# Performance work log

Hardware: AMD Instinct MI355X
Metric: run time of the kernel (lower is better)

Reference implementation:

```python
import jax, jax.numpy as jnp
import numpy as np

V, D, H, L, S_MAX = 32000, 1024, 16, 4, 1024
HD = D // H          # head dim = 64
FF = 4 * D           # mlp hidden = 4096
B, S = 2, 1024


def _layernorm(x, w, b, eps=1e-5):
    mu = jnp.mean(x, axis=-1, keepdims=True)
    var = jnp.mean(jnp.square(x - mu), axis=-1, keepdims=True)
    return (x - mu) * jax.lax.rsqrt(var + eps) * w + b


def setup_inputs() -> dict:
    key = jax.random.key(0)
    ks = jax.random.split(key, 16)
    r = lambda k, shape: (jax.random.normal(k, shape, dtype=jnp.float32) * 0.02)
    return {
        "input_ids": jax.random.randint(ks[0], (B, S), 0, V),
        "tok_emb": r(ks[1], (V, D)),
        "pos_emb": r(ks[2], (S_MAX, D)),
        "ln1_w": jnp.ones((L, D)), "ln1_b": jnp.zeros((L, D)),
        "ln2_w": jnp.ones((L, D)), "ln2_b": jnp.zeros((L, D)),
        "q_w": r(ks[3], (L, D, D)), "q_b": jnp.zeros((L, D)),
        "k_w": r(ks[4], (L, D, D)), "k_b": jnp.zeros((L, D)),
        "v_w": r(ks[5], (L, D, D)), "v_b": jnp.zeros((L, D)),
        "o_w": r(ks[6], (L, D, D)), "o_b": jnp.zeros((L, D)),
        "fc1_w": r(ks[7], (L, FF, D)), "fc1_b": jnp.zeros((L, FF)),
        "fc2_w": r(ks[8], (L, D, FF)), "fc2_b": jnp.zeros((L, D)),
        "lnf_w": jnp.ones((D,)), "lnf_b": jnp.zeros((D,)),
        "head_w": r(ks[9], (V, D)),
    }


def reference(input_ids, tok_emb, pos_emb, ln1_w, ln1_b, ln2_w, ln2_b,
              q_w, q_b, k_w, k_b, v_w, v_b, o_w, o_b,
              fc1_w, fc1_b, fc2_w, fc2_b, lnf_w, lnf_b, head_w):
    b, s = input_ids.shape
    x = tok_emb[input_ids] + pos_emb[:s][None, :, :]          # [B,S,D]
    causal = jnp.tril(jnp.ones((s, s), dtype=bool))           # [S,S]
    scale = 1.0 / np.sqrt(HD)
    for i in range(L):
        # --- causal MHA block ---
        h = _layernorm(x, ln1_w[i], ln1_b[i])
        q = (h @ q_w[i].T + q_b[i]).reshape(b, s, H, HD)
        k = (h @ k_w[i].T + k_b[i]).reshape(b, s, H, HD)
        v = (h @ v_w[i].T + v_b[i]).reshape(b, s, H, HD)
        scores = jnp.einsum('bqhd,bkhd->bhqk', q, k) * scale  # [B,H,S,S]
        scores = jnp.where(causal[None, None], scores, -jnp.inf)
        attn = jax.nn.softmax(scores, axis=-1)
        y = jnp.einsum('bhqk,bkhd->bqhd', attn, v).reshape(b, s, D)
        x = x + (y @ o_w[i].T + o_b[i])
        # --- GELU MLP block (exact gelu, matching torch F.gelu default) ---
        h = _layernorm(x, ln2_w[i], ln2_b[i])
        h = jax.nn.gelu(h @ fc1_w[i].T + fc1_b[i], approximate=False)
        x = x + (h @ fc2_w[i].T + fc2_b[i])
    x = _layernorm(x, lnf_w, lnf_b)
    logits = x[:, -1, :] @ head_w.T                           # [B,V]
    return logits
```

## Files before the change

kernel.cpp:

```cpp
#include <hip/hip_runtime.h>

#define V_SIZE 32000
#define D_DIM  1024
#define H_HEADS 16
#define L_LAYERS 4
#define HD_DIM 64
#define FF_DIM 4096
#define B_BATCH 2
#define S_SEQ  1024
#define M_ROWS (B_BATCH*S_SEQ)
#define KSPL   2

typedef short  s16x8 __attribute__((ext_vector_type(8)));
typedef unsigned short u16x8 __attribute__((ext_vector_type(8)));
typedef float  f32x4 __attribute__((ext_vector_type(4)));
typedef unsigned short u16;
typedef unsigned int   u32;

__device__ inline u16 f2bf(float f){
    u32 u = __float_as_uint(f);
    return (u16)((u + 0x7FFFu + ((u >> 16) & 1u)) >> 16);
}
__device__ inline float b2f(u32 v){ return __uint_as_float(v << 16); }

__device__ inline float gelu_f(float v){
    float y = 0.7978845608f * (v + 0.044715f*v*v*v);
    y = fmaxf(-15.f, fminf(15.f, y));
    float u = __expf(-2.f*y);
    return v / (1.f + u);
}

__device__ inline char* lds_swz(void* base, int row, int byteoff){
    return (char*)base + row*128 + (byteoff ^ ((row & 7) << 4));
}

__device__ inline void gload16(const u16* g, u16* l){
    __builtin_amdgcn_global_load_lds(
        (const __attribute__((address_space(1))) void*)g,
        (__attribute__((address_space(3))) void*)l, 16, 0, 0);
}

__device__ inline int swz_src_col(int lin){
    int row = lin >> 3, s8 = lin & 7;
    return (s8*8) ^ ((row & 7) << 3);
}

__device__ inline s16x8 cvt8(float4 a, float4 b){
    s16x8 o;
    o[0]=(short)f2bf(a.x); o[1]=(short)f2bf(a.y);
    o[2]=(short)f2bf(a.z); o[3]=(short)f2bf(a.w);
    o[4]=(short)f2bf(b.x); o[5]=(short)f2bf(b.y);
    o[6]=(short)f2bf(b.z); o[7]=(short)f2bf(b.w);
    return o;
}

__global__ __launch_bounds__(256) void cvt_all_k(
    const float* __restrict__ qw, const float* __restrict__ kw,
    const float* __restrict__ vw, const float* __restrict__ ow,
    const float* __restrict__ f1w, const float* __restrict__ f2w,
    u16* __restrict__ w_qkv, u16* __restrict__ w_o,
    u16* __restrict__ w_f1, u16* __restrict__ w_f2)
{
    const long M1 = 1L << 20;
    const int bx = blockIdx.x;
    const float* s; u16* d; long base;
    if (bx < 3072){
        int which = bx >> 10;
        s = (which==0) ? qw : ((which==1) ? kw : vw);
        base = (long)(bx & 1023) * 4096;
        long layer = base >> 20, rem = base & (M1 - 1);
        d = w_qkv + layer*3*M1 + which*M1 + rem;
        s += base;
    } else if (bx < 4096){
        base = (long)(bx - 3072) * 4096; s = ow  + base; d = w_o  + base;
    } else if (bx < 8192){
        base = (long)(bx - 4096) * 4096; s = f1w + base; d = w_f1 + base;
    } else {
        base = (long)(bx - 8192) * 4096; s = f2w + base; d = w_f2 + base;
    }
    const int t8 = threadIdx.x * 8;
#pragma unroll
    for (int j = 0; j < 2; j++){
        const float* sp = s + j*2048 + t8;
        float4 v0 = *(const float4*)(sp);
        float4 v1 = *(const float4*)(sp + 4);
        *(s16x8*)(d + j*2048 + t8) = cvt8(v0, v1);
    }
}

__global__ __launch_bounds__(256) void embed_ln_k(
    const int* __restrict__ ids, const float* __restrict__ tok,
    const float* __restrict__ pos, const float* __restrict__ lw,
    const float* __restrict__ lb, float* __restrict__ x, u16* __restrict__ h)
{
    int row = blockIdx.x;
    int id  = ids[row];
    int s   = row & (S_SEQ - 1);
    int t   = threadIdx.x;
    float4 tv = *(const float4*)(tok + (size_t)id * D_DIM + t*4);
    float4 pv = *(const float4*)(pos + (size_t)s  * D_DIM + t*4);
    float4 vv;
    vv.x = tv.x + pv.x; vv.y = tv.y + pv.y; vv.z = tv.z + pv.z; vv.w = tv.w + pv.w;
    *(float4*)(x + (size_t)row * D_DIM + t*4) = vv;
    float sm  = vv.x + vv.y + vv.z + vv.w;
    float ss = vv.x*vv.x + vv.y*vv.y + vv.z*vv.z + vv.w*vv.w;
#pragma unroll
    for (int off = 1; off < 64; off <<= 1){
        sm += __shfl_xor(sm, off);
        ss += __shfl_xor(ss, off);
    }
    __shared__ float red[8];
    const int wid = t >> 6, lane = t & 63;
    if (lane == 0){ red[wid] = sm; red[4 + wid] = ss; }
    __syncthreads();
    sm = red[0] + red[1] + red[2] + red[3];
    ss = red[4] + red[5] + red[6] + red[7];
    float mu   = sm * (1.0f/1024.0f);
    float rstd = rsqrtf(ss * (1.0f/1024.0f) - mu*mu + 1e-5f);
    float4 wv = *(const float4*)(lw + t*4);
    float4 bv = *(const float4*)(lb + t*4);
    uint2 pk;
    pk.x = (u32)f2bf((vv.x-mu)*rstd*wv.x + bv.x) | ((u32)f2bf((vv.y-mu)*rstd*wv.y + bv.y) << 16);
    pk.y = (u32)f2bf((vv.z-mu)*rstd*wv.z + bv.z) | ((u32)f2bf((vv.w-mu)*rstd*wv.w + bv.w) << 16);
    *(uint2*)(h + (size_t)row * D_DIM + t*4) = pk;
}

__global__ __launch_bounds__(256) void ln_k(
    const float* __restrict__ x, const float* __restrict__ lw,
    const float* __restrict__ lb, u16* __restrict__ h)
{
    const int row = blockIdx.x, t = threadIdx.x;
    float4 a = *(const float4*)(x + (size_t)row * D_DIM + t*4);
    float sm = a.x + a.y + a.z + a.w;
    float ss = a.x*a.x + a.y*a.y + a.z*a.z + a.w*a.w;
#pragma unroll
    for (int o2 = 1; o2 < 64; o2 <<= 1){
        sm += __shfl_xor(sm, o2);
        ss += __shfl_xor(ss, o2);
    }
    __shared__ float red[8];
    const int wid = t >> 6, lane = t & 63;
    if (lane == 0){ red[wid] = sm; red[4 + wid] = ss; }
    __syncthreads();
    sm = red[0] + red[1] + red[2] + red[3];
    ss = red[4] + red[5] + red[6] + red[7];
    float mu   = sm * (1.0f/1024.0f);
    float rstd = rsqrtf(ss * (1.0f/1024.0f) - mu*mu + 1e-5f);
    float4 wv  = *(const float4*)(lw + t*4);
    float4 lbv = *(const float4*)(lb + t*4);
    uint2 pk;
    pk.x = (u32)f2bf((a.x-mu)*rstd*wv.x + lbv.x) | ((u32)f2bf((a.y-mu)*rstd*wv.y + lbv.y) << 16);
    pk.y = (u32)f2bf((a.z-mu)*rstd*wv.z + lbv.z) | ((u32)f2bf((a.w-mu)*rstd*wv.w + lbv.w) << 16);
    *(uint2*)(h + (size_t)row * D_DIM + t*4) = pk;
}

__global__ __launch_bounds__(256) void ln_pair_f_k(
    const float* __restrict__ x2, const float* __restrict__ w, const float* __restrict__ bb,
    float* __restrict__ outF)
{
    const int row = blockIdx.x, t = threadIdx.x;
    float4 vv = *(const float4*)(x2 + (size_t)row * D_DIM + t*4);
    float s  = vv.x + vv.y + vv.z + vv.w;
    float ss = vv.x*vv.x + vv.y*vv.y + vv.z*vv.z + vv.w*vv.w;
#pragma unroll
    for (int off = 1; off < 64; off <<= 1){
        s  += __shfl_xor(s,  off);
        ss += __shfl_xor(ss, off);
    }
    __shared__ float red[8];
    const int wid = t >> 6, lane = t & 63;
    if (lane == 0){ red[wid] = s; red[4 + wid] = ss; }
    __syncthreads();
    s  = red[0] + red[1] + red[2] + red[3];
    ss = red[4] + red[5] + red[6] + red[7];
    float mu   = s * (1.0f/1024.0f);
    float rstd = rsqrtf(ss * (1.0f/1024.0f) - mu*mu + 1e-5f);
    float4 wv = *(const float4*)(w  + t*4);
    float4 bv = *(const float4*)(bb + t*4);
    float4 o;
    o.x = (vv.x - mu)*rstd*wv.x + bv.x;
    o.y = (vv.y - mu)*rstd*wv.y + bv.y;
    o.z = (vv.z - mu)*rstd*wv.z + bv.z;
    o.w = (vv.w - mu)*rstd*wv.w + bv.w;
    *(float4*)(outF + (size_t)row * D_DIM + t*4) = o;
}

__global__ __launch_bounds__(256) void reduce_ln_k(
    const u16* __restrict__ part, const float* __restrict__ bias,
    float* __restrict__ x,
    const float* __restrict__ lw, const float* __restrict__ lb,
    u16* __restrict__ h)
{
    const int row = blockIdx.x, t = threadIdx.x;
    const size_t off = (size_t)row * D_DIM + t*4;
    float4 a = *(float4*)(x + off);
    float4 bv = *(const float4*)(bias + t*4);
    a.x += bv.x; a.y += bv.y; a.z += bv.z; a.w += bv.w;
#pragma unroll
    for (int si = 0; si < KSPL; si++){
        uint2 pv = *(const uint2*)(part + (size_t)si * M_ROWS * D_DIM + off);
        a.x += b2f(pv.x & 0xffffu); a.y += b2f(pv.x >> 16);
        a.z += b2f(pv.y & 0xffffu); a.w += b2f(pv.y >> 16);
    }
    *(float4*)(x + off) = a;
    float sm = a.x + a.y + a.z + a.w;
    float ss = a.x*a.x + a.y*a.y + a.z*a.z + a.w*a.w;
#pragma unroll
    for (int o2 = 1; o2 < 64; o2 <<= 1){
        sm += __shfl_xor(sm, o2);
        ss += __shfl_xor(ss, o2);
    }
    __shared__ float red[8];
    const int wid = t >> 6, lane = t & 63;
    if (lane == 0){ red[wid] = sm; red[4 + wid] = ss; }
    __syncthreads();
    sm = red[0] + red[1] + red[2] + red[3];
    ss = red[4] + red[5] + red[6] + red[7];
    float mu   = sm * (1.0f/1024.0f);
    float rstd = rsqrtf(ss * (1.0f/1024.0f) - mu*mu + 1e-5f);
    float4 wv = *(const float4*)(lw + t*4);
    float4 lbv = *(const float4*)(lb + t*4);
    uint2 pk;
    pk.x = (u32)f2bf((a.x-mu)*rstd*wv.x + lbv.x) | ((u32)f2bf((a.y-mu)*rstd*wv.y + lbv.y) << 16);
    pk.y = (u32)f2bf((a.z-mu)*rstd*wv.z + lbv.z) | ((u32)f2bf((a.w-mu)*rstd*wv.w + lbv.w) << 16);
    *(uint2*)(h + (size_t)row * D_DIM + t*4) = pk;
}

__global__ __launch_bounds__(256) void gemm_fc1_k(
    const u16* __restrict__ A, const u16* __restrict__ Bw,
    const float* __restrict__ b0, u16* __restrict__ outB, int Ndim, int Kdim)
{
    const int nx = gridDim.x, ny = gridDim.y;
    const int nwg = nx*ny;
    int orig = blockIdx.y*nx + blockIdx.x;
    int wg = (orig & 7)*(nwg >> 3) + (orig >> 3);
    const int bm = wg % nx;
    const int bn = wg / nx;

    const int nk = Kdim >> 6;

    __shared__ __align__(16) u16 As[2][128*64];
    __shared__ __align__(16) u16 Bs[2][128*64];

    const int t = threadIdx.x;
    const int wid = t >> 6, lane = t & 63, lr = lane & 15, lg = lane >> 4;
    const int wr = wid >> 1, wc = wid & 1;

    f32x4 acc[4][4];
#pragma unroll
    for (int m=0;m<4;m++)
#pragma unroll
        for (int n=0;n<4;n++) acc[m][n] = (f32x4){0.f,0.f,0.f,0.f};

    const u16* Abase = A  + (size_t)(bm*128)*Kdim;
    const u16* Bbase = Bw + (size_t)(bn*128)*Kdim;

    auto stage = [&](int koff, int buf){
#pragma unroll
        for (int i=0;i<4;i++){
            int lin = i*256 + t;
            int row = lin >> 3;
            int sc  = swz_src_col(lin);
            gload16(Abase + (size_t)row*Kdim + koff + sc, &As[buf][lin*8]);
        }
#pragma unroll
        for (int i=0;i<4;i++){
            int lin = i*256 + t;
            int row = lin >> 3;
            int sc  = swz_src_col(lin);
            gload16(Bbase + (size_t)row*Kdim + koff + sc, &Bs[buf][lin*8]);
        }
    };

    stage(0, 0);
    __syncthreads();
    int cb = 0;
    for (int ki = 0; ki < nk; ki++){
        if (ki+1 < nk) stage((ki+1)*64, cb^1);
#pragma unroll
        for (int kk=0;kk<2;kk++){
            s16x8 a[4], b[4];
#pragma unroll
            for (int m=0;m<4;m++)
                a[m] = *(s16x8*)lds_swz(As[cb], wr*64 + m*16 + lr, kk*64 + lg*16);
#pragma unroll
            for (int n=0;n<4;n++)
                b[n] = *(s16x8*)lds_swz(Bs[cb], wc*64 + n*16 + lr, kk*64 + lg*16);
#pragma unroll
            for (int m=0;m<4;m++)
#pragma unroll
                for (int n=0;n<4;n++)
                    acc[m][n] = __builtin_amdgcn_mfma_f32_16x16x32_bf16(a[m], b[n], acc[m][n], 0, 0, 0);
        }
        __syncthreads();
        cb ^= 1;
    }

#pragma unroll
    for (int n=0;n<4;n++){
        int col = bn*128 + wc*64 + n*16 + lr;
        float bvv = b0[col];
#pragma unroll
        for (int m=0;m<4;m++){
            int row0 = bm*128 + wr*64 + m*16 + lg*4;
#pragma unroll
            for (int j=0;j<4;j++){
                int row = row0 + j;
                float val = gelu_f(acc[m][n][j] + bvv);
                outB[(size_t)row * Ndim + col] = f2bf(val);
            }
        }
    }
}

__global__ __launch_bounds__(256) void gemm_qkv_k(
    const u16* __restrict__ A, const u16* __restrict__ Bw,
    const float* __restrict__ b0, const float* __restrict__ b1, const float* __restrict__ b2,
    u16* __restrict__ outB, int Ndim, int Kdim)
{
    const int nx = gridDim.x, ny = gridDim.y;
    const int nwg = nx*ny;
    int orig = blockIdx.y*nx + blockIdx.x;
    int wg = (orig & 7)*(nwg >> 3) + (orig >> 3);
    const int bm = wg % nx;
    const int bn = wg / nx;
    const int nk = Kdim >> 6;

    __shared__ __align__(16) u16 As[2][64*64];
    __shared__ __align__(16) u16 Bs[2][128*64];

    const int t = threadIdx.x;
    const int wid = t >> 6, lane = t & 63, lr = lane & 15, lg = lane >> 4;
    const int wr = wid >> 1, wc = wid & 1;

    f32x4 acc[2][4];
#pragma unroll
    for (int m=0;m<2;m++)
#pragma unroll
        for (int n=0;n<4;n++) acc[m][n] = (f32x4){0.f,0.f,0.f,0.f};

    const u16* Abase = A  + (size_t)(bm*64)*Kdim;
    const u16* Bbase = Bw + (size_t)(bn*128)*Kdim;

    auto stage = [&](int koff, int buf){
#pragma unroll
        for (int i=0;i<2;i++){
            int lin = i*256 + t;
            int row = lin >> 3;
            int sc  = swz_src_col(lin);
            gload16(Abase + (size_t)row*Kdim + koff + sc, &As[buf][lin*8]);
        }
#pragma unroll
        for (int i=0;i<4;i++){
            int lin = i*256 + t;
            int row = lin >> 3;
            int sc  = swz_src_col(lin);
            gload16(Bbase + (size_t)row*Kdim + koff + sc, &Bs[buf][lin*8]);
        }
    };

    stage(0, 0);
    __syncthreads();
    int cb = 0;
    for (int ki = 0; ki < nk; ki++){
        if (ki+1 < nk) stage((ki+1)*64, cb^1);
#pragma unroll
        for (int kk=0;kk<2;kk++){
            s16x8 a[2], b[4];
#pragma unroll
            for (int m=0;m<2;m++)
                a[m] = *(s16x8*)lds_swz(As[cb], wr*32 + m*16 + lr, kk*64 + lg*16);
#pragma unroll
            for (int n=0;n<4;n++)
                b[n] = *(s16x8*)lds_swz(Bs[cb], wc*64 + n*16 + lr, kk*64 + lg*16);
#pragma unroll
            for (int m=0;m<2;m++)
#pragma unroll
                for (int n=0;n<4;n++)
                    acc[m][n] = __builtin_amdgcn_mfma_f32_16x16x32_bf16(a[m], b[n], acc[m][n], 0, 0, 0);
        }
        __syncthreads();
        cb ^= 1;
    }

#pragma unroll
    for (int n=0;n<4;n++){
        int col = bn*128 + wc*64 + n*16 + lr;
        int which = col >> 10;
        const float* bp = (which==0) ? b0 : ((which==1) ? b1 : b2);
        float bvv = bp[col & 1023];
        float scl = (which == 0) ? 0.125f : 1.0f;
#pragma unroll
        for (int m=0;m<2;m++){
            int row0 = bm*64 + wr*32 + m*16 + lg*4;
#pragma unroll
            for (int j=0;j<4;j++){
                int row = row0 + j;
                float val = (acc[m][n][j] + bvv) * scl;
                outB[(size_t)row * Ndim + col] = f2bf(val);
            }
        }
    }
}

__global__ __launch_bounds__(256) void gemm64_k(
    const u16* __restrict__ A, const u16* __restrict__ Bw,
    u16* __restrict__ outP, int Ndim, int Kdim, int kper)
{
    const int nx = gridDim.x, ny = gridDim.y;
    const int nwg = nx*ny*gridDim.z;
    int orig = (blockIdx.z*ny + blockIdx.y)*nx + blockIdx.x;
    int wg = (orig & 7)*(nwg >> 3) + (orig >> 3);
    const int bm = wg % nx; wg /= nx;
    const int bn = wg % ny;
    const int z  = wg / ny;
    const int kbeg = z * kper;
    const int nk = kper >> 6;

    __shared__ __align__(16) u16 As[2][64*64];
    __shared__ __align__(16) u16 Bs[2][128*64];

    const int t = threadIdx.x;
    const int wid = t >> 6, lane = t & 63, lr = lane & 15, lg = lane >> 4;
    const int wr = wid >> 1, wc = wid & 1;

    f32x4 acc[2][4];
#pragma unroll
    for (int m=0;m<2;m++)
#pragma unroll
        for (int n=0;n<4;n++) acc[m][n] = (f32x4){0.f,0.f,0.f,0.f};

    const u16* Abase = A  + (size_t)(bm*64)*Kdim + kbeg;
    const u16* Bbase = Bw + (size_t)(bn*128)*Kdim + kbeg;

    auto stage = [&](int koff, int buf){
#pragma unroll
        for (int i=0;i<2;i++){
            int lin = i*256 + t;
            int row = lin >> 3;
            int sc  = swz_src_col(lin);
            gload16(Abase + (size_t)row*Kdim + koff + sc, &As[buf][lin*8]);
        }
#pragma unroll
        for (int i=0;i<4;i++){
            int lin = i*256 + t;
            int row = lin >> 3;
            int sc  = swz_src_col(lin);
            gload16(Bbase + (size_t)row*Kdim + koff + sc, &Bs[buf][lin*8]);
        }
    };

    stage(0, 0);
    __syncthreads();
    int cb = 0;
    for (int ki = 0; ki < nk; ki++){
        if (ki+1 < nk) stage((ki+1)*64, cb^1);
#pragma unroll
        for (int kk=0;kk<2;kk++){
            s16x8 a[2], b[4];
#pragma unroll
            for (int m=0;m<2;m++)
                a[m] = *(s16x8*)lds_swz(As[cb], wr*32 + m*16 + lr, kk*64 + lg*16);
#pragma unroll
            for (int n=0;n<4;n++)
                b[n] = *(s16x8*)lds_swz(Bs[cb], wc*64 + n*16 + lr, kk*64 + lg*16);
#pragma unroll
            for (int m=0;m<2;m++)
#pragma unroll
                for (int n=0;n<4;n++)
                    acc[m][n] = __builtin_amdgcn_mfma_f32_16x16x32_bf16(a[m], b[n], acc[m][n], 0, 0, 0);
        }
        __syncthreads();
        cb ^= 1;
    }

#pragma unroll
    for (int n=0;n<4;n++){
        int col = bn*128 + wc*64 + n*16 + lr;
#pragma unroll
        for (int m=0;m<2;m++){
            int row0 = bm*64 + wr*32 + m*16 + lg*4;
#pragma unroll
            for (int j=0;j<4;j++){
                int row = row0 + j;
                outP[(size_t)z * M_ROWS * Ndim + (size_t)row * Ndim + col] = f2bf(acc[m][n][j]);
            }
        }
    }
}

__global__ __launch_bounds__(256) void attn_k(
    const u16* __restrict__ qkv, u16* __restrict__ y)
{
    const int gx = gridDim.x;
    const int nwg = gx * gridDim.y;
    int orig = blockIdx.y*gx + blockIdx.x;
    int wg = (orig & 7)*(nwg >> 3) + (orig >> 3);
    const int p  = wg % gx;
    const int bh = wg / gx;
    const int b  = bh >> 4, h = bh & 15;

    const int s_lo = p, s_hi = 15 - p;
    const int ntiles = s_hi + 1;

    __shared__ __align__(16) u16 Ks[2][64*64];
    __shared__ __align__(16) u16 VTs[2][64*64];
    __shared__ __align__(16) u16 Ps[4][16*64];

    const int t = threadIdx.x, wid = t >> 6, lane = t & 63, lr = lane & 15, lg = lane >> 4;
    const size_t rowb = (size_t)b * S_SEQ;
    const u16* qp = qkv + h*HD_DIM;
    const u16* kp = qkv + 1024 + h*HD_DIM;
    const u16* vp = qkv + 2048 + h*HD_DIM;

    const int qw_lo = s_lo*64 + wid*16;
    const int qw_hi = s_hi*64 + wid*16;

    s16x8 aq_lo[2], aq_hi[2];
#pragma unroll
    for (int kc=0;kc<2;kc++){
        aq_lo[kc] = *(const s16x8*)(qp + (rowb + qw_lo + lr) * 3072 + kc*32 + lg*8);
        aq_hi[kc] = *(const s16x8*)(qp + (rowb + qw_hi + lr) * 3072 + kc*32 + lg*8);
    }

    f32x4 o_lo[4], o_hi[4];
#pragma unroll
    for (int n=0;n<4;n++){ o_lo[n] = (f32x4){0.f,0.f,0.f,0.f}; o_hi[n] = (f32x4){0.f,0.f,0.f,0.f}; }
    float l_lo[4] = {0.f,0.f,0.f,0.f}, l_hi[4] = {0.f,0.f,0.f,0.f};

    const int kpr = t >> 3, dsl = t & 7;
    u16x8 vr0, vr1;

    auto issueK = [&](int kt, int buf){
#pragma unroll
        for (int i=0;i<2;i++){
            int lin = i*256 + t;
            int row = lin >> 3;
            int sc  = swz_src_col(lin);
            gload16(kp + (rowb + kt*64 + row)*3072 + sc, &Ks[buf][lin*8]);
        }
    };
    auto loadV = [&](int kt){
        vr0 = *(const u16x8*)(vp + (rowb + kt*64 + 2*kpr    )*3072 + dsl*8);
        vr1 = *(const u16x8*)(vp + (rowb + kt*64 + 2*kpr + 1)*3072 + dsl*8);
    };
    auto writeVT = [&](int buf){
#pragma unroll
        for (int j=0;j<8;j++){
            u32 pk = (u32)vr0[j] | ((u32)vr1[j] << 16);
            *(u32*)lds_swz(VTs[buf], dsl*8 + j, kpr*4) = pk;
        }
    };

    auto doStrip = [&](const s16x8* aq, f32x4* o, float* lsum, int qwS, int kt, bool diag, int cb){
        f32x4 sf[4];
#pragma unroll
        for (int n=0;n<4;n++) sf[n] = (f32x4){0.f,0.f,0.f,0.f};
        __builtin_amdgcn_s_setprio(1);
#pragma unroll
        for (int kc=0;kc<2;kc++){
#pragma unroll
            for (int n=0;n<4;n++){
                s16x8 bk = *(s16x8*)lds_swz(Ks[cb], n*16 + lr, kc*64 + lg*16);
                sf[n] = __builtin_amdgcn_mfma_f32_16x16x32_bf16(aq[kc], bk, sf[n], 0, 0, 0);
            }
        }
        __builtin_amdgcn_s_setprio(0);
        float rs[4] = {0.f,0.f,0.f,0.f};
#pragma unroll
        for (int n=0;n<4;n++){
            int key = kt*64 + n*16 + lr;
#pragma unroll
            for (int j=0;j<4;j++){
                float pe = __expf(sf[n][j]);
                if (diag && key > qwS + lg*4 + j) pe = 0.f;
                sf[n][j] = pe; rs[j] += pe;
            }
        }
#pragma unroll
        for (int off=1; off<16; off<<=1){
#pragma unroll
            for (int j=0;j<4;j++) rs[j] += __shfl_xor(rs[j], off);
        }
#pragma unroll
        for (int j=0;j<4;j++) lsum[j] += rs[j];
        u16* Pw = Ps[wid];
#pragma unroll
        for (int n=0;n<4;n++)
#pragma unroll
            for (int j=0;j<4;j++)
                *(u16*)lds_swz(Pw, lg*4 + j, (n*16 + lr)*2) = f2bf(sf[n][j]);
        __builtin_amdgcn_s_setprio(1);
#pragma unroll
        for (int kc=0;kc<2;kc++){
            s16x8 pa = *(s16x8*)lds_swz(Pw, lr, kc*64 + lg*16);
#pragma unroll
            for (int n=0;n<4;n++){
                s16x8 bv = *(s16x8*)lds_swz(VTs[cb], n*16 + lr, kc*64 + lg*16);
                o[n] = __builtin_amdgcn_mfma_f32_16x16x32_bf16(pa, bv, o[n], 0, 0, 0);
            }
        }
        __builtin_amdgcn_s_setprio(0);
    };

    issueK(0, 0); loadV(0); writeVT(0);
    __syncthreads();
    int cb = 0;
    for (int kt = 0; kt < ntiles; kt++){
        const bool more = (kt+1 < ntiles);
        if (more){ issueK(kt+1, cb^1); loadV(kt+1); }

        doStrip(aq_hi, o_hi, l_hi, qw_hi, kt, kt == s_hi, cb);
        if (kt <= s_lo)
            doStrip(aq_lo, o_lo, l_lo, qw_lo, kt, kt == s_lo, cb);

        if (more) writeVT(cb^1);
        __syncthreads();
        cb ^= 1;
    }

    float inv_lo[4], inv_hi[4];
#pragma unroll
    for (int j=0;j<4;j++){ inv_lo[j] = 1.0f / l_lo[j]; inv_hi[j] = 1.0f / l_hi[j]; }
#pragma unroll
    for (int n=0;n<4;n++)
#pragma unroll
        for (int j=0;j<4;j++){
            y[(rowb + qw_hi + lg*4 + j) * D_DIM + h*HD_DIM + n*16 + lr] = f2bf(o_hi[n][j] * inv_hi[j]);
            y[(rowb + qw_lo + lg*4 + j) * D_DIM + h*HD_DIM + n*16 + lr] = f2bf(o_lo[n][j] * inv_lo[j]);
        }
}

__global__ __launch_bounds__(256) void attn_last_k(
    const u16* __restrict__ qkv, float* __restrict__ Yp, float* __restrict__ psp)
{
    const int chunk = blockIdx.x;
    const int bh = blockIdx.y;
    const int b = bh >> 4, h = bh & 15;
    const int t = threadIdx.x;
    const size_t rowb = (size_t)b * S_SEQ;
    const size_t qrow = rowb + S_SEQ - 1;
    __shared__ float qs[64];
    __shared__ float ps[256];
    __shared__ float red[4];
    __shared__ float yred[4][64];
    if (t < 64) qs[t] = b2f(qkv[qrow*3072 + h*HD_DIM + t]);
    __syncthreads();
    int k = chunk*256 + t;
    const u16* krow = qkv + (rowb + k)*3072 + 1024 + h*HD_DIM;
    float s = 0.f;
#pragma unroll
    for (int j=0;j<8;j++){
        u16x8 kv = *(const u16x8*)(krow + j*8);
#pragma unroll
        for (int e=0;e<8;e++) s += qs[j*8+e] * b2f((u32)(unsigned short)kv[e]);
    }
    float p = __expf(s);
    ps[t] = p;
    float sp_ = p;
#pragma unroll
    for (int off=1; off<64; off<<=1) sp_ += __shfl_xor(sp_, off);
    if ((t & 63) == 0) red[t>>6] = sp_;
    __syncthreads();
    if (t == 0) psp[chunk*32 + bh] = red[0]+red[1]+red[2]+red[3];
    int d = t & 63, c = t >> 6;
    float acc = 0.f;
    const u16* vbase = qkv + (rowb + chunk*256 + c*64)*3072 + 2048 + h*HD_DIM + d;
    for (int kk=0; kk<64; kk++)
        acc += ps[c*64 + kk] * b2f((u32)vbase[(size_t)kk*3072]);
    yred[c][d] = acc;
    __syncthreads();
    if (t < 64)
        Yp[(chunk*32 + bh)*64 + t] = yred[0][t]+yred[1][t]+yred[2][t]+yred[3][t];
}

__global__ __launch_bounds__(64) void attn_comb_k(
    const float* __restrict__ Yp, const float* __restrict__ psp, u16* __restrict__ y2)
{
    int bh = blockIdx.x, t = threadIdx.x;
    float psum = psp[bh] + psp[32+bh] + psp[64+bh] + psp[96+bh];
    float y = Yp[bh*64+t] + Yp[(32+bh)*64+t] + Yp[(64+bh)*64+t] + Yp[(96+bh)*64+t];
    int b = bh >> 4, h = bh & 15;
    y2[b*1024 + h*64 + t] = f2bf(y / psum);
}

template<int MODE>
__global__ __launch_bounds__(256) void rowpair_k(
    const u16* __restrict__ A2, const u16* __restrict__ W,
    const float* __restrict__ bias, const float* __restrict__ xin,
    float* __restrict__ outF, u16* __restrict__ outB,
    int Ndim, int Kdim)
{
    const int t = threadIdx.x, wid = t >> 6, lane = t & 63;
    const int colsPerBlock = Ndim >> 8;
    const int colsPerWave  = colsPerBlock >> 2;
    const int nj = Kdim >> 9;
    for (int cc = 0; cc < colsPerWave; cc++){
        int col = blockIdx.x * colsPerBlock + wid * colsPerWave + cc;
        const u16* wrow = W + (size_t)col * Kdim;
        float s0 = 0.f, s1 = 0.f;
        for (int j = 0; j < nj; j++){
            int k = j*512 + lane*8;
            u16x8 wv = *(const u16x8*)(wrow + k);
            u16x8 a0 = *(const u16x8*)(A2 + k);
            u16x8 a1 = *(const u16x8*)(A2 + Kdim + k);
#pragma unroll
            for (int e=0;e<8;e++){
                float wf = b2f((u32)wv[e]);
                s0 += b2f((u32)a0[e]) * wf;
                s1 += b2f((u32)a1[e]) * wf;
            }
        }
#pragma unroll
        for (int off=1; off<64; off<<=1){
            s0 += __shfl_xor(s0, off);
            s1 += __shfl_xor(s1, off);
        }
        if (lane == 0){
            float bv = bias[col];
            if (MODE == 0){
                outF[col]         = xin[(size_t)(S_SEQ-1)*D_DIM + col]   + bv + s0;
                outF[D_DIM + col] = xin[(size_t)(2*S_SEQ-1)*D_DIM + col] + bv + s1;
            } else if (MODE == 1){
                outB[col]         = f2bf(gelu_f(s0 + bv));
                outB[Ndim + col]  = f2bf(gelu_f(s1 + bv));
            } else {
                outF[col]         = xin[col]         + bv + s0;
                outF[D_DIM + col] = xin[D_DIM + col] + bv + s1;
            }
        }
    }
}

__global__ __launch_bounds__(256) void head_k(
    const float* __restrict__ xf, const float* __restrict__ hw, float* __restrict__ out)
{
    __shared__ float xs[2*D_DIM];
    int t = threadIdx.x;
#pragma unroll
    for (int i=0;i<2;i++){
        int j = t + i*256;
        *(float4*)&xs[j*4] = *(const float4*)(xf + j*4);
    }
    __syncthreads();
    int wid = t >> 6, lane = t & 63;
    int vrow = blockIdx.x * 4 + wid;
    float s0 = 0.f, s1 = 0.f;
#pragma unroll
    for (int it=0; it<4; it++){
        int j = it*64 + lane;
        float4 w4 = *(const float4*)(hw + (size_t)vrow * D_DIM + j*4);
        float4 x0 = *(const float4*)&xs[j*4];
        float4 x1 = *(const float4*)&xs[D_DIM + j*4];
        s0 += w4.x*x0.x + w4.y*x0.y + w4.z*x0.z + w4.w*x0.w;
        s1 += w4.x*x1.x + w4.y*x1.y + w4.z*x1.z + w4.w*x1.w;
    }
#pragma unroll
    for (int off=1; off<64; off<<=1){
        s0 += __shfl_xor(s0, off);
        s1 += __shfl_xor(s1, off);
    }
    if (lane == 0){
        out[vrow]          = s0;
        out[V_SIZE + vrow] = s1;
    }
}

extern "C" void kernel_launch(void* const* d_in, const int* in_sizes, int n_in,
                              void* d_out, int out_size, void* d_ws, size_t ws_size,
                              hipStream_t stream)
{
    (void)in_sizes; (void)n_in; (void)out_size; (void)ws_size;
    const int*   ids  = (const int*)  d_in[0];
    const float* tok  = (const float*)d_in[1];
    const float* pos  = (const float*)d_in[2];
    const float* ln1w = (const float*)d_in[3];
    const float* ln1b = (const float*)d_in[4];
    const float* ln2w = (const float*)d_in[5];
    const float* ln2b = (const float*)d_in[6];
    const float* qw   = (const float*)d_in[7];
    const float* qbi  = (const float*)d_in[8];
    const float* kw   = (const float*)d_in[9];
    const float* kbi  = (const float*)d_in[10];
    const float* vw   = (const float*)d_in[11];
    const float* vbi  = (const float*)d_in[12];
    const float* ow   = (const float*)d_in[13];
    const float* obi  = (const float*)d_in[14];
    const float* f1w  = (const float*)d_in[15];
    const float* f1b  = (const float*)d_in[16];
    const float* f2w  = (const float*)d_in[17];
    const float* f2b  = (const float*)d_in[18];
    const float* lnfw = (const float*)d_in[19];
    const float* lnfb = (const float*)d_in[20];
    const float* hw   = (const float*)d_in[21];

    const long MD = (long)1024*1024;
    char* p = (char*)d_ws;
    float* x    = (float*)p; p += (size_t)M_ROWS * D_DIM * 4;
    u16* h      = (u16*)p;   p += (size_t)M_ROWS * D_DIM * 2;
    u16* qkvbuf = (u16*)p;   p += (size_t)M_ROWS * 3072 * 2;
    u16* ybuf   = (u16*)p;   p += (size_t)M_ROWS * D_DIM * 2;
    u16* h1     = (u16*)p;   p += (size_t)M_ROWS * FF_DIM * 2;
    u16* part   = (u16*)p;   p += (size_t)KSPL * M_ROWS * D_DIM * 2;
    u16* wbuf   = (u16*)p;   p += (size_t)48 * MD * 2;
    float* xf   = (float*)p; p += 2 * D_DIM * 4;
    u16*   y2   = (u16*)p;   p += 2 * D_DIM * 2;
    float* x2   = (float*)p; p += 2 * D_DIM * 4;
    float* x3   = (float*)p; p += 2 * D_DIM * 4;
    u16*   h2   = (u16*)p;   p += 2 * D_DIM * 2;
    u16*   g2   = (u16*)p;   p += 2 * FF_DIM * 2;
    float* Yp   = (float*)p; p += 4 * 32 * 64 * 4;
    float* psp  = (float*)p; p += 4 * 32 * 4;
    float* logits = (float*)d_out;

    u16* w_qkv = wbuf;
    u16* w_o   = wbuf + 12*MD;
    u16* w_f1  = wbuf + 16*MD;
    u16* w_f2  = wbuf + 32*MD;

    cvt_all_k<<<dim3(12288), 256, 0, stream>>>(
        qw, kw, vw, ow, f1w, f2w, w_qkv, w_o, w_f1, w_f2);

    embed_ln_k<<<dim3(M_ROWS), 256, 0, stream>>>(ids, tok, pos, ln1w, ln1b, x, h);

    for (int i = 0; i < L_LAYERS - 1; i++){
        gemm_qkv_k<<<dim3(32, 24), 256, 0, stream>>>(
            h, w_qkv + (size_t)i*3*MD,
            qbi + i*D_DIM, kbi + i*D_DIM, vbi + i*D_DIM,
            qkvbuf, 3072, D_DIM);
        attn_k<<<dim3(8, 32), 256, 0, stream>>>(qkvbuf, ybuf);
        gemm64_k<<<dim3(32, 8, KSPL), 256, 0, stream>>>(
            ybuf, w_o + (size_t)i*MD, part, D_DIM, D_DIM, D_DIM/KSPL);
        reduce_ln_k<<<dim3(M_ROWS), 256, 0, stream>>>(
            part, obi + i*D_DIM, x, ln2w + i*D_DIM, ln2b + i*D_DIM, h);
        gemm_fc1_k<<<dim3(16, 32), 256, 0, stream>>>(
            h, w_f1 + (size_t)i*4*MD, f1b + i*FF_DIM, h1, FF_DIM, D_DIM);
        gemm64_k<<<dim3(32, 8, KSPL), 256, 0, stream>>>(
            h1, w_f2 + (size_t)i*4*MD, part, D_DIM, FF_DIM, FF_DIM/KSPL);
        reduce_ln_k<<<dim3(M_ROWS), 256, 0, stream>>>(
            part, f2b + i*D_DIM, x, ln1w + (i+1)*D_DIM, ln1b + (i+1)*D_DIM, h);
    }

    const int L3 = L_LAYERS - 1;
    gemm_qkv_k<<<dim3(32, 24), 256, 0, stream>>>(
        h, w_qkv + (size_t)L3*3*MD,
        qbi + L3*D_DIM, kbi + L3*D_DIM, vbi + L3*D_DIM,
        qkvbuf, 3072, D_DIM);
    attn_last_k<<<dim3(4, 32), 256, 0, stream>>>(qkvbuf, Yp, psp);
    attn_comb_k<<<dim3(32), 64, 0, stream>>>(Yp, psp, y2);
    rowpair_k<0><<<dim3(256), 256, 0, stream>>>(
        y2, w_o + (size_t)L3*MD, obi + L3*D_DIM, x, x2, nullptr, D_DIM, D_DIM);
    ln_k<<<dim3(2), 256, 0, stream>>>(x2, ln2w + L3*D_DIM, ln2b + L3*D_DIM, h2);
    rowpair_k<1><<<dim3(256), 256, 0, stream>>>(
        h2, w_f1 + (size_t)L3*4*MD, f1b + L3*FF_DIM, nullptr, nullptr, g2, FF_DIM, D_DIM);
    rowpair_k<2><<<dim3(256), 256, 0, stream>>>(
        g2, w_f2 + (size_t)L3*4*MD, f2b + L3*D_DIM, x2, x3, nullptr, D_DIM, FF_DIM);
    ln_pair_f_k<<<dim3(2), 256, 0, stream>>>(x3, lnfw, lnfb, xf);

    head_k<<<dim3(V_SIZE/4), 256, 0, stream>>>(xf, hw, logits);
}
```

Baseline: 533.6 us.

## Fuse last-layer small kernels and compute only K/V for final layer

Removes the separate ln_k, attn_comb_k and ln_pair_f_k kernels by folding their work into the rowpair and head kernels. The head kernel now recomputes the final layernorm for both rows in every block. The final layer's QKV GEMM now computes only K and V, and Q for the two last rows comes from a rowpair GEMV. FC1 now uses the templated 64-row-tile GEMM instead of the 128x128 kernel. This cuts launches and skips most of the final-layer Q projection, at the cost of redundant per-block layernorm work in the head kernel.

```diff
diff --git a/kernel.cpp b/kernel.cpp
--- a/kernel.cpp
+++ b/kernel.cpp
@@ -125,66 +125,6 @@
     *(uint2*)(h + (size_t)row * D_DIM + t*4) = pk;
 }
 
-__global__ __launch_bounds__(256) void ln_k(
-    const float* __restrict__ x, const float* __restrict__ lw,
-    const float* __restrict__ lb, u16* __restrict__ h)
-{
-    const int row = blockIdx.x, t = threadIdx.x;
-    float4 a = *(const float4*)(x + (size_t)row * D_DIM + t*4);
-    float sm = a.x + a.y + a.z + a.w;
-    float ss = a.x*a.x + a.y*a.y + a.z*a.z + a.w*a.w;
-#pragma unroll
-    for (int o2 = 1; o2 < 64; o2 <<= 1){
-        sm += __shfl_xor(sm, o2);
-        ss += __shfl_xor(ss, o2);
-    }
-    __shared__ float red[8];
-    const int wid = t >> 6, lane = t & 63;
-    if (lane == 0){ red[wid] = sm; red[4 + wid] = ss; }
-    __syncthreads();
-    sm = red[0] + red[1] + red[2] + red[3];
-    ss = red[4] + red[5] + red[6] + red[7];
-    float mu   = sm * (1.0f/1024.0f);
-    float rstd = rsqrtf(ss * (1.0f/1024.0f) - mu*mu + 1e-5f);
-    float4 wv  = *(const float4*)(lw + t*4);
-    float4 lbv = *(const float4*)(lb + t*4);
-    uint2 pk;
-    pk.x = (u32)f2bf((a.x-mu)*rstd*wv.x + lbv.x) | ((u32)f2bf((a.y-mu)*rstd*wv.y + lbv.y) << 16);
-    pk.y = (u32)f2bf((a.z-mu)*rstd*wv.z + lbv.z) | ((u32)f2bf((a.w-mu)*rstd*wv.w + lbv.w) << 16);
-    *(uint2*)(h + (size_t)row * D_DIM + t*4) = pk;
-}
-
-__global__ __launch_bounds__(256) void ln_pair_f_k(
-    const float* __restrict__ x2, const float* __restrict__ w, const float* __restrict__ bb,
-    float* __restrict__ outF)
-{
-    const int row = blockIdx.x, t = threadIdx.x;
-    float4 vv = *(const float4*)(x2 + (size_t)row * D_DIM + t*4);
-    float s  = vv.x + vv.y + vv.z + vv.w;
-    float ss = vv.x*vv.x + vv.y*vv.y + vv.z*vv.z + vv.w*vv.w;
-#pragma unroll
-    for (int off = 1; off < 64; off <<= 1){
-        s  += __shfl_xor(s,  off);
-        ss += __shfl_xor(ss, off);
-    }
-    __shared__ float red[8];
-    const int wid = t >> 6, lane = t & 63;
-    if (lane == 0){ red[wid] = s; red[4 + wid] = ss; }
-    __syncthreads();
-    s  = red[0] + red[1] + red[2] + red[3];
-    ss = red[4] + red[5] + red[6] + red[7];
-    float mu   = s * (1.0f/1024.0f);
-    float rstd = rsqrtf(ss * (1.0f/1024.0f) - mu*mu + 1e-5f);
-    float4 wv = *(const float4*)(w  + t*4);
-    float4 bv = *(const float4*)(bb + t*4);
-    float4 o;
-    o.x = (vv.x - mu)*rstd*wv.x + bv.x;
-    o.y = (vv.y - mu)*rstd*wv.y + bv.y;
-    o.z = (vv.z - mu)*rstd*wv.z + bv.z;
-    o.w = (vv.w - mu)*rstd*wv.w + bv.w;
-    *(float4*)(outF + (size_t)row * D_DIM + t*4) = o;
-}
-
 __global__ __launch_bounds__(256) void reduce_ln_k(
     const u16* __restrict__ part, const float* __restrict__ bias,
     float* __restrict__ x,
@@ -226,94 +166,8 @@
     *(uint2*)(h + (size_t)row * D_DIM + t*4) = pk;
 }
 
-__global__ __launch_bounds__(256) void gemm_fc1_k(
-    const u16* __restrict__ A, const u16* __restrict__ Bw,
-    const float* __restrict__ b0, u16* __restrict__ outB, int Ndim, int Kdim)
-{
-    const int nx = gridDim.x, ny = gridDim.y;
-    const int nwg = nx*ny;
-    int orig = blockIdx.y*nx + blockIdx.x;
-    int wg = (orig & 7)*(nwg >> 3) + (orig >> 3);
-    const int bm = wg % nx;
-    const int bn = wg / nx;
-
-    const int nk = Kdim >> 6;
-
-    __shared__ __align__(16) u16 As[2][128*64];
-    __shared__ __align__(16) u16 Bs[2][128*64];
-
-    const int t = threadIdx.x;
-    const int wid = t >> 6, lane = t & 63, lr = lane & 15, lg = lane >> 4;
-    const int wr = wid >> 1, wc = wid & 1;
-
-    f32x4 acc[4][4];
-#pragma unroll
-    for (int m=0;m<4;m++)
-#pragma unroll
-        for (int n=0;n<4;n++) acc[m][n] = (f32x4){0.f,0.f,0.f,0.f};
-
-    const u16* Abase = A  + (size_t)(bm*128)*Kdim;
-    const u16* Bbase = Bw + (size_t)(bn*128)*Kdim;
-
-    auto stage = [&](int koff, int buf){
-#pragma unroll
-        for (int i=0;i<4;i++){
-            int lin = i*256 + t;
-            int row = lin >> 3;
-            int sc  = swz_src_col(lin);
-            gload16(Abase + (size_t)row*Kdim + koff + sc, &As[buf][lin*8]);
-        }
-#pragma unroll
-        for (int i=0;i<4;i++){
-            int lin = i*256 + t;
-            int row = lin >> 3;
-            int sc  = swz_src_col(lin);
-            gload16(Bbase + (size_t)row*Kdim + koff + sc, &Bs[buf][lin*8]);
-        }
-    };
-
-    stage(0, 0);
-    __syncthreads();
-    int cb = 0;
-    for (int ki = 0; ki < nk; ki++){
-        if (ki+1 < nk) stage((ki+1)*64, cb^1);
-#pragma unroll
-        for (int kk=0;kk<2;kk++){
-            s16x8 a[4], b[4];
-#pragma unroll
-            for (int m=0;m<4;m++)
-                a[m] = *(s16x8*)lds_swz(As[cb], wr*64 + m*16 + lr, kk*64 + lg*16);
-#pragma unroll
-            for (int n=0;n<4;n++)
-                b[n] = *(s16x8*)lds_swz(Bs[cb], wc*64 + n*16 + lr, kk*64 + lg*16);
-#pragma unroll
-            for (int m=0;m<4;m++)
-#pragma unroll
-                for (int n=0;n<4;n++)
-                    acc[m][n] = __builtin_amdgcn_mfma_f32_16x16x32_bf16(a[m], b[n], acc[m][n], 0, 0, 0);
-        }
-        __syncthreads();
-        cb ^= 1;
-    }
-
-#pragma unroll
-    for (int n=0;n<4;n++){
-        int col = bn*128 + wc*64 + n*16 + lr;
-        float bvv = b0[col];
-#pragma unroll
-        for (int m=0;m<4;m++){
-            int row0 = bm*128 + wr*64 + m*16 + lg*4;
-#pragma unroll
-            for (int j=0;j<4;j++){
-                int row = row0 + j;
-                float val = gelu_f(acc[m][n][j] + bvv);
-                outB[(size_t)row * Ndim + col] = f2bf(val);
-            }
-        }
-    }
-}
-
-__global__ __launch_bounds__(256) void gemm_qkv_k(
+template<int EPI, int QSEG>
+__global__ __launch_bounds__(256) void gemm64o_k(
     const u16* __restrict__ A, const u16* __restrict__ Bw,
     const float* __restrict__ b0, const float* __restrict__ b1, const float* __restrict__ b2,
     u16* __restrict__ outB, int Ndim, int Kdim)
@@ -386,17 +240,24 @@
 #pragma unroll
     for (int n=0;n<4;n++){
         int col = bn*128 + wc*64 + n*16 + lr;
-        int which = col >> 10;
-        const float* bp = (which==0) ? b0 : ((which==1) ? b1 : b2);
-        float bvv = bp[col & 1023];
-        float scl = (which == 0) ? 0.125f : 1.0f;
+        float bvv, scl = 1.0f;
+        if (EPI == 1){
+            bvv = b0[col];
+        } else {
+            int which = col >> 10;
+            const float* bp = (which==0) ? b0 : ((which==1) ? b1 : b2);
+            bvv = bp[col & 1023];
+            if (which == QSEG) scl = 0.125f;
+        }
 #pragma unroll
         for (int m=0;m<2;m++){
             int row0 = bm*64 + wr*32 + m*16 + lg*4;
 #pragma unroll
             for (int j=0;j<4;j++){
                 int row = row0 + j;
-                float val = (acc[m][n][j] + bvv) * scl;
+                float val = acc[m][n][j] + bvv;
+                if (EPI == 1) val = gelu_f(val);
+                else          val *= scl;
                 outB[(size_t)row * Ndim + col] = f2bf(val);
             }
         }
@@ -632,28 +493,28 @@
 }
 
 __global__ __launch_bounds__(256) void attn_last_k(
-    const u16* __restrict__ qkv, float* __restrict__ Yp, float* __restrict__ psp)
+    const u16* __restrict__ q2, const u16* __restrict__ kv,
+    float* __restrict__ Yp, float* __restrict__ psp)
 {
     const int chunk = blockIdx.x;
     const int bh = blockIdx.y;
     const int b = bh >> 4, h = bh & 15;
     const int t = threadIdx.x;
     const size_t rowb = (size_t)b * S_SEQ;
-    const size_t qrow = rowb + S_SEQ - 1;
     __shared__ float qs[64];
     __shared__ float ps[256];
     __shared__ float red[4];
     __shared__ float yred[4][64];
-    if (t < 64) qs[t] = b2f(qkv[qrow*3072 + h*HD_DIM + t]);
+    if (t < 64) qs[t] = b2f(q2[b*1024 + h*HD_DIM + t]);
     __syncthreads();
     int k = chunk*256 + t;
-    const u16* krow = qkv + (rowb + k)*3072 + 1024 + h*HD_DIM;
+    const u16* krow = kv + (rowb + k)*2048 + h*HD_DIM;
     float s = 0.f;
 #pragma unroll
     for (int j=0;j<8;j++){
-        u16x8 kv = *(const u16x8*)(krow + j*8);
-#pragma unroll
-        for (int e=0;e<8;e++) s += qs[j*8+e] * b2f((u32)(unsigned short)kv[e]);
+        u16x8 kv8 = *(const u16x8*)(krow + j*8);
+#pragma unroll
+        for (int e=0;e<8;e++) s += qs[j*8+e] * b2f((u32)(unsigned short)kv8[e]);
     }
     float p = __expf(s);
     ps[t] = p;
@@ -665,33 +526,70 @@
     if (t == 0) psp[chunk*32 + bh] = red[0]+red[1]+red[2]+red[3];
     int d = t & 63, c = t >> 6;
     float acc = 0.f;
-    const u16* vbase = qkv + (rowb + chunk*256 + c*64)*3072 + 2048 + h*HD_DIM + d;
+    const u16* vbase = kv + (rowb + chunk*256 + c*64)*2048 + 1024 + h*HD_DIM + d;
     for (int kk=0; kk<64; kk++)
-        acc += ps[c*64 + kk] * b2f((u32)vbase[(size_t)kk*3072]);
+        acc += ps[c*64 + kk] * b2f((u32)vbase[(size_t)kk*2048]);
     yred[c][d] = acc;
     __syncthreads();
     if (t < 64)
         Yp[(chunk*32 + bh)*64 + t] = yred[0][t]+yred[1][t]+yred[2][t]+yred[3][t];
 }
 
-__global__ __launch_bounds__(64) void attn_comb_k(
-    const float* __restrict__ Yp, const float* __restrict__ psp, u16* __restrict__ y2)
-{
-    int bh = blockIdx.x, t = threadIdx.x;
-    float psum = psp[bh] + psp[32+bh] + psp[64+bh] + psp[96+bh];
-    float y = Yp[bh*64+t] + Yp[(32+bh)*64+t] + Yp[(64+bh)*64+t] + Yp[(96+bh)*64+t];
-    int b = bh >> 4, h = bh & 15;
-    y2[b*1024 + h*64 + t] = f2bf(y / psum);
-}
-
 template<int MODE>
 __global__ __launch_bounds__(256) void rowpair_k(
-    const u16* __restrict__ A2, const u16* __restrict__ W,
-    const float* __restrict__ bias, const float* __restrict__ xin,
+    const u16* __restrict__ A0, const u16* __restrict__ A1,
+    const float* __restrict__ Yp, const float* __restrict__ psp,
+    const float* __restrict__ x2in,
+    const float* __restrict__ lw, const float* __restrict__ lb,
+    const u16* __restrict__ W, const float* __restrict__ bias,
+    const float* __restrict__ xresid,
     float* __restrict__ outF, u16* __restrict__ outB,
     int Ndim, int Kdim)
 {
+    __shared__ u16 As16[2][1024];
+    __shared__ float red[8];
     const int t = threadIdx.x, wid = t >> 6, lane = t & 63;
+
+    if (MODE == 0){
+        for (int idx = t; idx < 2048; idx += 256){
+            int r = idx >> 10, d10 = idx & 1023;
+            int bh = r*16 + (d10 >> 6), d = d10 & 63;
+            float psum = psp[bh] + psp[32+bh] + psp[64+bh] + psp[96+bh];
+            float yv = Yp[bh*64+d] + Yp[(32+bh)*64+d] + Yp[(64+bh)*64+d] + Yp[(96+bh)*64+d];
+            As16[r][d10] = f2bf(yv / psum);
+        }
+        __syncthreads();
+    }
+    if (MODE == 1){
+#pragma unroll
+        for (int r = 0; r < 2; r++){
+            float4 vv = *(const float4*)(x2in + r*1024 + t*4);
+            float sm = vv.x + vv.y + vv.z + vv.w;
+            float ss = vv.x*vv.x + vv.y*vv.y + vv.z*vv.z + vv.w*vv.w;
+#pragma unroll
+            for (int o2 = 1; o2 < 64; o2 <<= 1){
+                sm += __shfl_xor(sm, o2);
+                ss += __shfl_xor(ss, o2);
+            }
+            if (lane == 0){ red[wid] = sm; red[4+wid] = ss; }
+            __syncthreads();
+            sm = red[0]+red[1]+red[2]+red[3];
+            ss = red[4]+red[5]+red[6]+red[7];
+            float mu = sm * (1.0f/1024.0f);
+            float rstd = rsqrtf(ss * (1.0f/1024.0f) - mu*mu + 1e-5f);
+            float4 wv  = *(const float4*)(lw + t*4);
+            float4 lbv = *(const float4*)(lb + t*4);
+            As16[r][t*4+0] = f2bf((vv.x-mu)*rstd*wv.x + lbv.x);
+            As16[r][t*4+1] = f2bf((vv.y-mu)*rstd*wv.y + lbv.y);
+            As16[r][t*4+2] = f2bf((vv.z-mu)*rstd*wv.z + lbv.z);
+            As16[r][t*4+3] = f2bf((vv.w-mu)*rstd*wv.w + lbv.w);
+            __syncthreads();
+        }
+    }
+
+    const u16* pa0 = (MODE==0 || MODE==1) ? (const u16*)As16[0] : A0;
+    const u16* pa1 = (MODE==0 || MODE==1) ? (const u16*)As16[1] : A1;
+
     const int colsPerBlock = Ndim >> 8;
     const int colsPerWave  = colsPerBlock >> 2;
     const int nj = Kdim >> 9;
@@ -702,8 +600,8 @@
         for (int j = 0; j < nj; j++){
             int k = j*512 + lane*8;
             u16x8 wv = *(const u16x8*)(wrow + k);
-            u16x8 a0 = *(const u16x8*)(A2 + k);
-            u16x8 a1 = *(const u16x8*)(A2 + Kdim + k);
+            u16x8 a0 = *(const u16x8*)(pa0 + k);
+            u16x8 a1 = *(const u16x8*)(pa1 + k);
 #pragma unroll
             for (int e=0;e<8;e++){
                 float wf = b2f((u32)wv[e]);
@@ -719,31 +617,53 @@
         if (lane == 0){
             float bv = bias[col];
             if (MODE == 0){
-                outF[col]         = xin[(size_t)(S_SEQ-1)*D_DIM + col]   + bv + s0;
-                outF[D_DIM + col] = xin[(size_t)(2*S_SEQ-1)*D_DIM + col] + bv + s1;
+                outF[col]         = xresid[(size_t)(S_SEQ-1)*D_DIM + col]   + bv + s0;
+                outF[D_DIM + col] = xresid[(size_t)(2*S_SEQ-1)*D_DIM + col] + bv + s1;
             } else if (MODE == 1){
                 outB[col]         = f2bf(gelu_f(s0 + bv));
                 outB[Ndim + col]  = f2bf(gelu_f(s1 + bv));
+            } else if (MODE == 2){
+                outF[col]         = x2in[col]         + bv + s0;
+                outF[D_DIM + col] = x2in[D_DIM + col] + bv + s1;
             } else {
-                outF[col]         = xin[col]         + bv + s0;
-                outF[D_DIM + col] = xin[D_DIM + col] + bv + s1;
+                outB[col]         = f2bf((s0 + bv) * 0.125f);
+                outB[Ndim + col]  = f2bf((s1 + bv) * 0.125f);
             }
         }
     }
 }
 
-__global__ __launch_bounds__(256) void head_k(
-    const float* __restrict__ xf, const float* __restrict__ hw, float* __restrict__ out)
+__global__ __launch_bounds__(256) void head_ln_k(
+    const float* __restrict__ x3, const float* __restrict__ w, const float* __restrict__ bb,
+    const float* __restrict__ hw, float* __restrict__ out)
 {
     __shared__ float xs[2*D_DIM];
-    int t = threadIdx.x;
-#pragma unroll
-    for (int i=0;i<2;i++){
-        int j = t + i*256;
-        *(float4*)&xs[j*4] = *(const float4*)(xf + j*4);
-    }
-    __syncthreads();
-    int wid = t >> 6, lane = t & 63;
+    __shared__ float red[8];
+    int t = threadIdx.x, wid = t >> 6, lane = t & 63;
+#pragma unroll
+    for (int r = 0; r < 2; r++){
+        float4 vv = *(const float4*)(x3 + r*D_DIM + t*4);
+        float s  = vv.x + vv.y + vv.z + vv.w;
+        float ss = vv.x*vv.x + vv.y*vv.y + vv.z*vv.z + vv.w*vv.w;
+#pragma unroll
+        for (int off = 1; off < 64; off <<= 1){
+            s  += __shfl_xor(s,  off);
+            ss += __shfl_xor(ss, off);
+        }
+        if (lane == 0){ red[wid] = s; red[4+wid] = ss; }
+        __syncthreads();
+        s  = red[0]+red[1]+red[2]+red[3];
+        ss = red[4]+red[5]+red[6]+red[7];
+        float mu   = s * (1.0f/1024.0f);
+        float rstd = rsqrtf(ss * (1.0f/1024.0f) - mu*mu + 1e-5f);
+        float4 wv = *(const float4*)(w  + t*4);
+        float4 bv = *(const float4*)(bb + t*4);
+        xs[r*D_DIM + t*4+0] = (vv.x-mu)*rstd*wv.x + bv.x;
+        xs[r*D_DIM + t*4+1] = (vv.y-mu)*rstd*wv.y + bv.y;
+        xs[r*D_DIM + t*4+2] = (vv.z-mu)*rstd*wv.z + bv.z;
+        xs[r*D_DIM + t*4+3] = (vv.w-mu)*rstd*wv.w + bv.w;
+        __syncthreads();
+    }
     int vrow = blockIdx.x * 4 + wid;
     float s0 = 0.f, s1 = 0.f;
 #pragma unroll
@@ -803,11 +723,9 @@
     u16* h1     = (u16*)p;   p += (size_t)M_ROWS * FF_DIM * 2;
     u16* part   = (u16*)p;   p += (size_t)KSPL * M_ROWS * D_DIM * 2;
     u16* wbuf   = (u16*)p;   p += (size_t)48 * MD * 2;
-    float* xf   = (float*)p; p += 2 * D_DIM * 4;
-    u16*   y2   = (u16*)p;   p += 2 * D_DIM * 2;
+    u16*   q2   = (u16*)p;   p += 2 * D_DIM * 2;
     float* x2   = (float*)p; p += 2 * D_DIM * 4;
     float* x3   = (float*)p; p += 2 * D_DIM * 4;
-    u16*   h2   = (u16*)p;   p += 2 * D_DIM * 2;
     u16*   g2   = (u16*)p;   p += 2 * FF_DIM * 2;
     float* Yp   = (float*)p; p += 4 * 32 * 64 * 4;
     float* psp  = (float*)p; p += 4 * 32 * 4;
@@ -824,7 +742,7 @@
     embed_ln_k<<<dim3(M_ROWS), 256, 0, stream>>>(ids, tok, pos, ln1w, ln1b, x, h);
 
     for (int i = 0; i < L_LAYERS - 1; i++){
-        gemm_qkv_k<<<dim3(32, 24), 256, 0, stream>>>(
+        gemm64o_k<0,0><<<dim3(32, 24), 256, 0, stream>>>(
             h, w_qkv + (size_t)i*3*MD,
             qbi + i*D_DIM, kbi + i*D_DIM, vbi + i*D_DIM,
             qkvbuf, 3072, D_DIM);
@@ -833,8 +751,10 @@
             ybuf, w_o + (size_t)i*MD, part, D_DIM, D_DIM, D_DIM/KSPL);
         reduce_ln_k<<<dim3(M_ROWS), 256, 0, stream>>>(
             part, obi + i*D_DIM, x, ln2w + i*D_DIM, ln2b + i*D_DIM, h);
-        gemm_fc1_k<<<dim3(16, 32), 256, 0, stream>>>(
-            h, w_f1 + (size_t)i*4*MD, f1b + i*FF_DIM, h1, FF_DIM, D_DIM);
+        gemm64o_k<1,-1><<<dim3(32, 32), 256, 0, stream>>>(
+            h, w_f1 + (size_t)i*4*MD,
+            f1b + i*FF_DIM, nullptr, nullptr,
+            h1, FF_DIM, D_DIM);
         gemm64_k<<<dim3(32, 8, KSPL), 256, 0, stream>>>(
             h1, w_f2 + (size_t)i*4*MD, part, D_DIM, FF_DIM, FF_DIM/KSPL);
         reduce_ln_k<<<dim3(M_ROWS), 256, 0, stream>>>(
@@ -842,20 +762,28 @@
     }
 
     const int L3 = L_LAYERS - 1;
-    gemm_qkv_k<<<dim3(32, 24), 256, 0, stream>>>(
-        h, w_qkv + (size_t)L3*3*MD,
-        qbi + L3*D_DIM, kbi + L3*D_DIM, vbi + L3*D_DIM,
-        qkvbuf, 3072, D_DIM);
-    attn_last_k<<<dim3(4, 32), 256, 0, stream>>>(qkvbuf, Yp, psp);
-    attn_comb_k<<<dim3(32), 64, 0, stream>>>(Yp, psp, y2);
+    gemm64o_k<0,-1><<<dim3(32, 16), 256, 0, stream>>>(
+        h, w_qkv + (size_t)L3*3*MD + MD,
+        kbi + L3*D_DIM, vbi + L3*D_DIM, vbi + L3*D_DIM,
+        qkvbuf, 2048, D_DIM);
+    rowpair_k<3><<<dim3(256), 256, 0, stream>>>(
+        h + (size_t)(S_SEQ-1)*D_DIM, h + (size_t)(2*S_SEQ-1)*D_DIM,
+        nullptr, nullptr, nullptr, nullptr, nullptr,
+        w_qkv + (size_t)L3*3*MD, qbi + L3*D_DIM, nullptr,
+        nullptr, q2, D_DIM, D_DIM);
+    attn_last_k<<<dim3(4, 32), 256, 0, stream>>>(q2, qkvbuf, Yp, psp);
     rowpair_k<0><<<dim3(256), 256, 0, stream>>>(
-        y2, w_o + (size_t)L3*MD, obi + L3*D_DIM, x, x2, nullptr, D_DIM, D_DIM);
-    ln_k<<<dim3(2), 256, 0, stream>>>(x2, ln2w + L3*D_DIM, ln2b + L3*D_DIM, h2);
+        nullptr, nullptr, Yp, psp, nullptr, nullptr, nullptr,
+        w_o + (size_t)L3*MD, obi + L3*D_DIM, x,
+        x2, nullptr, D_DIM, D_DIM);
     rowpair_k<1><<<dim3(256), 256, 0, stream>>>(
-        h2, w_f1 + (size_t)L3*4*MD, f1b + L3*FF_DIM, nullptr, nullptr, g2, FF_DIM, D_DIM);
+        nullptr, nullptr, nullptr, nullptr, x2,
+        ln2w + L3*D_DIM, ln2b + L3*D_DIM,
+        w_f1 + (size_t)L3*4*MD, f1b + L3*FF_DIM, nullptr,
+        nullptr, g2, FF_DIM, D_DIM);
     rowpair_k<2><<<dim3(256), 256, 0, stream>>>(
-        g2, w_f2 + (size_t)L3*4*MD, f2b + L3*D_DIM, x2, x3, nullptr, D_DIM, FF_DIM);
-    ln_pair_f_k<<<dim3(2), 256, 0, stream>>>(x3, lnfw, lnfb, xf);
-
-    head_k<<<dim3(V_SIZE/4), 256, 0, stream>>>(xf, hw, logits);
-}
+        g2, g2 + FF_DIM, nullptr, nullptr, x2, nullptr, nullptr,
+        w_f2 + (size_t)L3*4*MD, f2b + L3*D_DIM, nullptr,
+        x3, nullptr, D_DIM, FF_DIM);
+    head_ln_k<<<dim3(V_SIZE/4), 256, 0, stream>>>(x3, lnfw, lnfb, hw, logits);
+}
```

Result: slower. 563.8 us (+5.7%).
